# Kernel optimization log

Measured on AMD Instinct MI355X. Metric: run time of the kernel, lower is better.

## Reference

```python
import jax, jax.numpy as jnp
import numpy as np

CLF_LAMBDA = 1.0
SCENARIO_SCALES = (1.0, 1.2)


def setup_inputs() -> dict:
    key = jax.random.key(0)
    ks = jax.random.split(key, 20)
    B, N, H, NC = 65536, 16, 128, 2
    s_in = 1.0 / np.sqrt(N)
    s_h = 1.0 / np.sqrt(H)
    return {
        "x": jax.random.normal(ks[0], (B, N), jnp.float32),
        "V1_w": jax.random.normal(ks[1], (H, N), jnp.float32) * s_in,
        "V1_b": jax.random.normal(ks[2], (H,), jnp.float32) * 0.1,
        "V2_w": jax.random.normal(ks[3], (H, H), jnp.float32) * s_h,
        "V2_b": jax.random.normal(ks[4], (H,), jnp.float32) * 0.1,
        "K1a_w": jax.random.normal(ks[5], (H, N), jnp.float32) * s_in,
        "K1a_b": jax.random.normal(ks[6], (H,), jnp.float32) * 0.1,
        "K1b_w": jax.random.normal(ks[7], (N, H), jnp.float32) * s_h,
        "K1b_b": jax.random.normal(ks[8], (N,), jnp.float32) * 0.1,
        "K2a_w": jax.random.normal(ks[9], (H, N), jnp.float32) * s_in,
        "K2a_b": jax.random.normal(ks[10], (H,), jnp.float32) * 0.1,
        "K2b_w": jax.random.normal(ks[11], (N, H), jnp.float32) * s_h,
        "K2b_b": jax.random.normal(ks[12], (N,), jnp.float32) * 0.1,
        "A_dyn": jax.random.normal(ks[13], (N, N), jnp.float32) * s_in,
        "B_dyn": jax.random.normal(ks[14], (N, NC), jnp.float32) * s_in,
        "x_goal": jax.random.normal(ks[15], (N,), jnp.float32),
        "u_eq": jax.random.normal(ks[16], (NC, 1), jnp.float32),
    }


def _forward(x, V1_w, V1_b, V2_w, V2_b, K1a_w, K1a_b, K1b_w, K1b_b,
             K2a_w, K2a_b, K2b_w, K2b_b, A_dyn, B_dyn, x_goal, u_eq):
    # --- Lyapunov value + manual Jacobian (diag_embed(1-t^2)@W == row-scaling) ---
    t1 = jnp.tanh(x @ V1_w.T + V1_b)                       # [B,H]
    t2 = jnp.tanh(t1 @ V2_w.T + V2_b)                      # [B,H]
    V = 0.5 * jnp.sum(t2 * t2, axis=1)                     # [B]
    D1 = (1.0 - t1 * t1)[:, :, None] * V1_w                # [B,H,N]
    # (diag(1-t2^2) @ V2_w) @ D1, contracted without materializing [B,H,H]
    D2 = jnp.einsum('bh,hk,bkn->bhn', 1.0 - t2 * t2, V2_w, D1)  # [B,H,N]
    grad_V = jnp.einsum('bh,bhn->bn', t2, D2)[:, None, :]  # [B,1,N]

    # --- learned gains K = stack(K1,K2); u = -K (x - x_goal) + u_eq ---
    K1 = jnp.tanh(x @ K1a_w.T + K1a_b) @ K1b_w.T + K1b_b   # [B,N]
    K2 = jnp.tanh(x @ K2a_w.T + K2a_b) @ K2b_w.T + K2b_b   # [B,N]
    K = jnp.stack((K1, K2), axis=1)                        # [B,2,N]
    dx = x - x_goal                                        # [B,N]
    u = -jnp.einsum('bcn,bn->bc', K, dx)[:, :, None] + u_eq  # [B,2,1]

    # --- CLF decrease condition per scenario (linear control-affine dynamics) ---
    gV = grad_V[:, 0, :]                                   # [B,N]
    L_g_V = gV @ B_dyn                                     # [B,NC] (g is state-indep)
    Vdot = jnp.zeros((x.shape[0], 1, 1), x.dtype)
    for scale in SCENARIO_SCALES:
        f = scale * (x @ A_dyn.T)                          # [B,N]
        L_f_V = jnp.sum(gV * f, axis=1)[:, None, None]     # [B,1,1]
        LgVu = jnp.einsum('bc,bco->bo', L_g_V, u)[:, :, None]  # [B,1,1]
        Vdot = Vdot + jax.nn.relu(L_f_V + LgVu + CLF_LAMBDA * V[:, None, None])
    Vdot = Vdot / len(SCENARIO_SCALES)
    relaxation = jnp.zeros((1,), x.dtype)
    return u, relaxation, V, Vdot


def reference(x, V1_w, V1_b, V2_w, V2_b, K1a_w, K1a_b, K1b_w, K1b_b,
              K2a_w, K2a_b, K2b_w, K2b_b, A_dyn, B_dyn, x_goal, u_eq):
    return _forward(x, V1_w, V1_b, V2_w, V2_b, K1a_w, K1a_b, K1b_w, K1b_b,
                    K2a_w, K2a_b, K2b_w, K2b_b, A_dyn, B_dyn, x_goal, u_eq)
```

## Files before the change

### kernel.cpp

```cpp
#include <hip/hip_runtime.h>


typedef __attribute__((ext_vector_type(8))) short bf8_t;
typedef __attribute__((ext_vector_type(4))) float f4_t;
typedef __attribute__((ext_vector_type(4))) short s4_t;

#define MFMA16(a, b, c) __builtin_amdgcn_mfma_f32_16x16x32_bf16((a), (b), (c), 0, 0, 0)

__device__ __forceinline__ float fast_tanh(float v) {
    float e = __builtin_amdgcn_exp2f(v * 2.885390081777927f);
    return 1.0f - 2.0f * __builtin_amdgcn_rcpf(e + 1.0f);
}
__device__ __forceinline__ unsigned short bf16_of(float f) {
    union { float f; unsigned u; } v; v.f = f;
    return (unsigned short)((v.u + 0x8000u) >> 16);
}
__device__ __forceinline__ unsigned pk2(float a, float b) {
    union { float f; unsigned u; } va, vb; va.f = a; vb.f = b;
    return ((va.u + 0x8000u) >> 16) | ((vb.u + 0x8000u) & 0xFFFF0000u);
}
__device__ __forceinline__ float unbf(unsigned short s) {
    union { unsigned u; float f; } v; v.u = ((unsigned)s) << 16; return v.f;
}

__global__ void prep_weights(const float* __restrict__ V1_w,
                             const float* __restrict__ V2_w,
                             const float* __restrict__ K1a_w,
                             const float* __restrict__ K1b_w,
                             const float* __restrict__ K2a_w,
                             const float* __restrict__ K2b_w,
                             const float* __restrict__ A_dyn,
                             unsigned short* __restrict__ ws) {
    int i = blockIdx.x * 256 + threadIdx.x;
    if (i < 2048) {
        ws[i] = bf16_of(V1_w[i]);
        int k = i & 127;
        ws[2048 + i] = bf16_of(V1_w[k * 16 + (i >> 7)]);
        ws[36864 + i] = bf16_of(K1a_w[i]);
        ws[38912 + i] = bf16_of(K2a_w[i]);
        ws[40960 + i] = bf16_of(K1b_w[i]);
        ws[43008 + i] = bf16_of(K2b_w[i]);
    }
    if (i < 16384) {
        ws[4096 + i] = bf16_of(V2_w[i]);
        int k = i >> 7, h = i & 127;
        ws[20480 + i] = bf16_of(V2_w[h * 128 + k]);
    }
    if (i < 256) ws[45056 + i] = bf16_of(A_dyn[i]);
}

__device__ __forceinline__ bf8_t pack8(f4_t a, f4_t b) {
    union { bf8_t v; unsigned u[4]; } r;
    r.u[0] = pk2(a[0], a[1]); r.u[1] = pk2(a[2], a[3]);
    r.u[2] = pk2(b[0], b[1]); r.u[3] = pk2(b[2], b[3]);
    return r.v;
}

__global__ void __launch_bounds__(512) clf_mfma_kernel(
    const float* __restrict__ x,
    const float* __restrict__ V1_b, const float* __restrict__ V2_b,
    const float* __restrict__ K1a_b, const float* __restrict__ K1b_b,
    const float* __restrict__ K2a_b, const float* __restrict__ K2b_b,
    const float* __restrict__ B_dyn, const float* __restrict__ x_goal,
    const float* __restrict__ u_eq,
    const unsigned short* __restrict__ ws, float* __restrict__ out, int B) {
    extern __shared__ unsigned short sm[];
    unsigned short* V2s  = sm;
    unsigned short* V2Ts = sm + 16384;
    unsigned short* V1Ts = sm + 32768;
    unsigned short* K1bs = sm + 34816;
    unsigned short* K2bs = sm + 36864;
    const int lane = threadIdx.x & 63;
    const int wv = threadIdx.x >> 6;
    const int lr = lane & 15;
    const int g = lane >> 4;
    const int bb = (blockIdx.x * 8 + wv) * 16 + lr;
    unsigned short* bufA = sm + 38912 + wv * 4096;
    unsigned short* bufB = bufA + 2048;

    if (blockIdx.x == 0 && threadIdx.x == 0) out[2 * B] = 0.0f;

#pragma unroll
    for (int q = 0; q < 4; ++q) {
        int e = (q * 512 + threadIdx.x) * 8;
        int r = e >> 7;
        int d = e ^ ((r & 7) << 3);
        *reinterpret_cast<uint4*>(&V2s[d])  = *reinterpret_cast<const uint4*>(ws + 4096 + e);
        *reinterpret_cast<uint4*>(&V2Ts[d]) = *reinterpret_cast<const uint4*>(ws + 20480 + e);
    }
    {
        int t3 = threadIdx.x;
        if (t3 < 256) {
            int e = t3 * 8; int r = e >> 7; int d = e ^ ((r & 7) << 3);
            *reinterpret_cast<uint4*>(&V1Ts[d]) = *reinterpret_cast<const uint4*>(ws + 2048 + e);
            *reinterpret_cast<uint4*>(&K2bs[d]) = *reinterpret_cast<const uint4*>(ws + 43008 + e);
        } else {
            int e = (t3 - 256) * 8; int r = e >> 7; int d = e ^ ((r & 7) << 3);
            *reinterpret_cast<uint4*>(&K1bs[d]) = *reinterpret_cast<const uint4*>(ws + 40960 + e);
        }
    }
    __syncthreads();

    const unsigned short* wsV1 = ws;
    const unsigned short* wsK1a = ws + 36864;
    const unsigned short* wsK2a = ws + 38912;
    const unsigned short* wsA = ws + 45056;

    const int swz = (lr & 7) << 3;
    auto stA = [&](unsigned short* buf, int h0, unsigned lo, unsigned hi) {
        int idx = (lr * 128 + h0) ^ swz;
        uint2 v; v.x = lo; v.y = hi;
        *reinterpret_cast<uint2*>(buf + idx) = v;
    };
    auto ld8 = [&](const unsigned short* buf, int h0) -> bf8_t {
        int idx = (lr * 128 + h0) ^ swz;
        return *reinterpret_cast<const bf8_t*>(buf + idx);
    };
    auto ld4 = [&](const unsigned short* buf, int h0) -> s4_t {
        int idx = (lr * 128 + h0) ^ swz;
        return *reinterpret_cast<const s4_t*>(buf + idx);
    };
    auto ldW = [&](const unsigned short* Wt, int t, int c) -> bf8_t {
        int idx = ((t * 16 + lr) * 128 + c * 32 + g * 8) ^ swz;
        return *reinterpret_cast<const bf8_t*>(Wt + idx);
    };
    auto ldK = [&](const unsigned short* Wt, int c) -> bf8_t {
        int idx = (lr * 128 + c * 32 + g * 8) ^ swz;
        return *reinterpret_cast<const bf8_t*>(Wt + idx);
    };

    bf8_t xf = {0, 0, 0, 0, 0, 0, 0, 0};
    if (g < 2) {
        const float* xp = x + bb * 16 + g * 8;
        f4_t a = *reinterpret_cast<const f4_t*>(xp);
        f4_t b = *reinterpret_cast<const f4_t*>(xp + 4);
        xf = pack8(a, b);
    }

    auto actnet = [&](const unsigned short* wsW, const float* bias, unsigned short* dst) {
#pragma unroll
        for (int t = 0; t < 8; ++t) {
            bf8_t af = {0, 0, 0, 0, 0, 0, 0, 0};
            if (g < 2) af = *reinterpret_cast<const bf8_t*>(wsW + (t * 16 + lr) * 16 + g * 8);
            f4_t acc = {0.f, 0.f, 0.f, 0.f};
            acc = MFMA16(af, xf, acc);
            f4_t bs = *reinterpret_cast<const f4_t*>(bias + t * 16 + g * 4);
            float v0 = fast_tanh(acc[0] + bs[0]);
            float v1 = fast_tanh(acc[1] + bs[1]);
            float v2 = fast_tanh(acc[2] + bs[2]);
            float v3 = fast_tanh(acc[3] + bs[3]);
            stA(dst, t * 16 + g * 4, pk2(v0, v1), pk2(v2, v3));
        }
    };
    auto ldfrag = [&](const unsigned short* buf, bf8_t (&f)[4]) {
        f[0] = ld8(buf, 0 + g * 8); f[1] = ld8(buf, 32 + g * 8);
        f[2] = ld8(buf, 64 + g * 8); f[3] = ld8(buf, 96 + g * 8);
    };
    auto kmul = [&](const unsigned short* Wt, const bf8_t (&f)[4]) -> f4_t {
        f4_t za = {0.f, 0.f, 0.f, 0.f}, zb = {0.f, 0.f, 0.f, 0.f};
        za = MFMA16(ldK(Wt, 0), f[0], za);
        zb = MFMA16(ldK(Wt, 1), f[1], zb);
        za = MFMA16(ldK(Wt, 2), f[2], za);
        zb = MFMA16(ldK(Wt, 3), f[3], zb);
        f4_t k;
        k[0] = za[0] + zb[0]; k[1] = za[1] + zb[1];
        k[2] = za[2] + zb[2]; k[3] = za[3] + zb[3];
        return k;
    };

    actnet(wsK1a, K1a_b, bufA);
    actnet(wsK2a, K2a_b, bufB);
    bf8_t fragA[4], fragB[4];
    ldfrag(bufA, fragA);
    ldfrag(bufB, fragB);
    f4_t k1 = kmul(K1bs, fragA);
    f4_t k2 = kmul(K2bs, fragB);

    actnet(wsV1, V1_b, bufA);
    bf8_t t1f[4];
    ldfrag(bufA, t1f);

    float vsum = 0.f;
#pragma unroll
    for (int t = 0; t < 8; ++t) {
        f4_t za = {0.f, 0.f, 0.f, 0.f}, zb = {0.f, 0.f, 0.f, 0.f};
        za = MFMA16(ldW(V2s, t, 0), t1f[0], za);
        zb = MFMA16(ldW(V2s, t, 1), t1f[1], zb);
        za = MFMA16(ldW(V2s, t, 2), t1f[2], za);
        zb = MFMA16(ldW(V2s, t, 3), t1f[3], zb);
        f4_t bs = *reinterpret_cast<const f4_t*>(V2_b + t * 16 + g * 4);
        float s0, s1, s2v, s3;
        {
            float t2;
            t2 = fast_tanh(za[0] + zb[0] + bs[0]); vsum = fmaf(t2, t2, vsum); s0 = t2 * (1.f - t2 * t2);
            t2 = fast_tanh(za[1] + zb[1] + bs[1]); vsum = fmaf(t2, t2, vsum); s1 = t2 * (1.f - t2 * t2);
            t2 = fast_tanh(za[2] + zb[2] + bs[2]); vsum = fmaf(t2, t2, vsum); s2v = t2 * (1.f - t2 * t2);
            t2 = fast_tanh(za[3] + zb[3] + bs[3]); vsum = fmaf(t2, t2, vsum); s3 = t2 * (1.f - t2 * t2);
        }
        stA(bufB, t * 16 + g * 4, pk2(s0, s1), pk2(s2v, s3));
    }
    bf8_t s2f[4];
    ldfrag(bufB, s2f);

#pragma unroll
    for (int t = 0; t < 8; ++t) {
        f4_t za = {0.f, 0.f, 0.f, 0.f}, zb = {0.f, 0.f, 0.f, 0.f};
        za = MFMA16(ldW(V2Ts, t, 0), s2f[0], za);
        zb = MFMA16(ldW(V2Ts, t, 1), s2f[1], zb);
        za = MFMA16(ldW(V2Ts, t, 2), s2f[2], za);
        zb = MFMA16(ldW(V2Ts, t, 3), s2f[3], zb);
        s4_t tv = ld4(bufA, t * 16 + g * 4);
        float t0v = unbf((unsigned short)tv[0]);
        float t1v = unbf((unsigned short)tv[1]);
        float t2v = unbf((unsigned short)tv[2]);
        float t3v = unbf((unsigned short)tv[3]);
        float c0 = (za[0] + zb[0]) * (1.f - t0v * t0v);
        float c1 = (za[1] + zb[1]) * (1.f - t1v * t1v);
        float c2 = (za[2] + zb[2]) * (1.f - t2v * t2v);
        float c3 = (za[3] + zb[3]) * (1.f - t3v * t3v);
        stA(bufB, t * 16 + g * 4, pk2(c0, c1), pk2(c2, c3));
    }
    bf8_t cf[4];
    ldfrag(bufB, cf);

    f4_t gacc = kmul(V1Ts, cf);

    bf8_t afA = {0, 0, 0, 0, 0, 0, 0, 0};
    if (g < 2) afA = *reinterpret_cast<const bf8_t*>(wsA + lr * 16 + g * 8);
    f4_t fz = {0.f, 0.f, 0.f, 0.f};
    f4_t fac = MFMA16(afA, xf, fz);

    f4_t xv = *reinterpret_cast<const f4_t*>(x + bb * 16 + g * 4);
    f4_t xg = *reinterpret_cast<const f4_t*>(x_goal + g * 4);
    f4_t k1b = *reinterpret_cast<const f4_t*>(K1b_b + g * 4);
    f4_t k2b = *reinterpret_cast<const f4_t*>(K2b_b + g * 4);
    f4_t bd0 = *reinterpret_cast<const f4_t*>(B_dyn + g * 8);
    f4_t bd1 = *reinterpret_cast<const f4_t*>(B_dyn + g * 8 + 4);
    float up0 = 0.f, up1 = 0.f, Lf = 0.f;
#pragma unroll
    for (int r = 0; r < 4; ++r) {
        float dx = xv[r] - xg[r];
        up0 = fmaf(k1[r] + k1b[r], dx, up0);
        up1 = fmaf(k2[r] + k2b[r], dx, up1);
        Lf = fmaf(gacc[r], fac[r], Lf);
    }
    float Lg0 = gacc[0] * bd0[0] + gacc[1] * bd0[2] + gacc[2] * bd1[0] + gacc[3] * bd1[2];
    float Lg1 = gacc[0] * bd0[1] + gacc[1] * bd0[3] + gacc[2] * bd1[1] + gacc[3] * bd1[3];
    up0 += __shfl_xor(up0, 16); up0 += __shfl_xor(up0, 32);
    up1 += __shfl_xor(up1, 16); up1 += __shfl_xor(up1, 32);
    Lf += __shfl_xor(Lf, 16); Lf += __shfl_xor(Lf, 32);
    Lg0 += __shfl_xor(Lg0, 16); Lg0 += __shfl_xor(Lg0, 32);
    Lg1 += __shfl_xor(Lg1, 16); Lg1 += __shfl_xor(Lg1, 32);
    vsum += __shfl_xor(vsum, 16); vsum += __shfl_xor(vsum, 32);

    float u0 = u_eq[0] - up0;
    float u1 = u_eq[1] - up1;
    float V = 0.5f * vsum;
    float G = fmaf(Lg0, u0, fmaf(Lg1, u1, V));
    float Vd = 0.5f * (fmaxf(Lf + G, 0.f) + fmaxf(fmaf(1.2f, Lf, G), 0.f));

    if (g == 0) {
        float2 uo; uo.x = u0; uo.y = u1;
        *reinterpret_cast<float2*>(out + 2 * bb) = uo;
    } else if (g == 1) {
        out[2 * B + 1 + bb] = V;
    } else if (g == 2) {
        out[3 * B + 1 + bb] = Vd;
    }
}

extern "C" void kernel_launch(void* const* d_in, const int* in_sizes, int n_in,
                              void* d_out, int out_size, void* d_ws, size_t ws_size,
                              hipStream_t stream) {
    const float* x = (const float*)d_in[0];
    const float* V1_w = (const float*)d_in[1];
    const float* V1_b = (const float*)d_in[2];
    const float* V2_w = (const float*)d_in[3];
    const float* V2_b = (const float*)d_in[4];
    const float* K1a_w = (const float*)d_in[5];
    const float* K1a_b = (const float*)d_in[6];
    const float* K1b_w = (const float*)d_in[7];
    const float* K1b_b = (const float*)d_in[8];
    const float* K2a_w = (const float*)d_in[9];
    const float* K2a_b = (const float*)d_in[10];
    const float* K2b_w = (const float*)d_in[11];
    const float* K2b_b = (const float*)d_in[12];
    const float* A_dyn = (const float*)d_in[13];
    const float* B_dyn = (const float*)d_in[14];
    const float* x_goal = (const float*)d_in[15];
    const float* u_eq = (const float*)d_in[16];
    float* out = (float*)d_out;
    unsigned short* ws = (unsigned short*)d_ws;

    const int B = in_sizes[0] / 16;
    const size_t smem = 143360;
    (void)hipFuncSetAttribute(reinterpret_cast<const void*>(clf_mfma_kernel),
                              hipFuncAttributeMaxDynamicSharedMemorySize, (int)smem);
    prep_weights<<<64, 256, 0, stream>>>(V1_w, V2_w, K1a_w, K1b_w, K2a_w, K2b_w, A_dyn, ws);
    clf_mfma_kernel<<<512, 512, smem, stream>>>(
        x, V1_b, V2_b, K1a_b, K1b_b, K2a_b, K2b_b,
        B_dyn, x_goal, u_eq, ws, out, B);
}
```

Baseline: 38.32 us.

## Use 11 waves per block and read small K/V1T weights from global

```diff
diff --git a/kernel.cpp b/kernel.cpp
--- a/kernel.cpp
+++ b/kernel.cpp
@@ -56,7 +56,7 @@
     return r.v;
 }
 
-__global__ void __launch_bounds__(512) clf_mfma_kernel(
+__global__ void __launch_bounds__(704) clf_mfma_kernel(
     const float* __restrict__ x,
     const float* __restrict__ V1_b, const float* __restrict__ V2_b,
     const float* __restrict__ K1a_b, const float* __restrict__ K1b_b,
@@ -67,43 +67,37 @@
     extern __shared__ unsigned short sm[];
     unsigned short* V2s  = sm;
     unsigned short* V2Ts = sm + 16384;
-    unsigned short* V1Ts = sm + 32768;
-    unsigned short* K1bs = sm + 34816;
-    unsigned short* K2bs = sm + 36864;
     const int lane = threadIdx.x & 63;
     const int wv = threadIdx.x >> 6;
     const int lr = lane & 15;
     const int g = lane >> 4;
-    const int bb = (blockIdx.x * 8 + wv) * 16 + lr;
-    unsigned short* bufA = sm + 38912 + wv * 4096;
+    const int wgid = blockIdx.x * 11 + wv;
+    const int bb = wgid * 16 + lr;
+    unsigned short* bufA = sm + 32768 + wv * 4096;
     unsigned short* bufB = bufA + 2048;
 
     if (blockIdx.x == 0 && threadIdx.x == 0) out[2 * B] = 0.0f;
 
 #pragma unroll
-    for (int q = 0; q < 4; ++q) {
-        int e = (q * 512 + threadIdx.x) * 8;
-        int r = e >> 7;
-        int d = e ^ ((r & 7) << 3);
-        *reinterpret_cast<uint4*>(&V2s[d])  = *reinterpret_cast<const uint4*>(ws + 4096 + e);
-        *reinterpret_cast<uint4*>(&V2Ts[d]) = *reinterpret_cast<const uint4*>(ws + 20480 + e);
-    }
-    {
-        int t3 = threadIdx.x;
-        if (t3 < 256) {
-            int e = t3 * 8; int r = e >> 7; int d = e ^ ((r & 7) << 3);
-            *reinterpret_cast<uint4*>(&V1Ts[d]) = *reinterpret_cast<const uint4*>(ws + 2048 + e);
-            *reinterpret_cast<uint4*>(&K2bs[d]) = *reinterpret_cast<const uint4*>(ws + 43008 + e);
-        } else {
-            int e = (t3 - 256) * 8; int r = e >> 7; int d = e ^ ((r & 7) << 3);
-            *reinterpret_cast<uint4*>(&K1bs[d]) = *reinterpret_cast<const uint4*>(ws + 40960 + e);
+    for (int q = 0; q < 3; ++q) {
+        int idx = q * 704 + threadIdx.x;
+        if (idx < 2048) {
+            int e = idx * 8;
+            int r = e >> 7;
+            int d = e ^ ((r & 7) << 3);
+            *reinterpret_cast<uint4*>(&V2s[d])  = *reinterpret_cast<const uint4*>(ws + 4096 + e);
+            *reinterpret_cast<uint4*>(&V2Ts[d]) = *reinterpret_cast<const uint4*>(ws + 20480 + e);
         }
     }
     __syncthreads();
+    if (wgid * 16 >= B) return;
 
     const unsigned short* wsV1 = ws;
+    const unsigned short* wsV1T = ws + 2048;
     const unsigned short* wsK1a = ws + 36864;
     const unsigned short* wsK2a = ws + 38912;
+    const unsigned short* wsK1b = ws + 40960;
+    const unsigned short* wsK2b = ws + 43008;
     const unsigned short* wsA = ws + 45056;
 
     const int swz = (lr & 7) << 3;
@@ -122,10 +116,6 @@
     };
     auto ldW = [&](const unsigned short* Wt, int t, int c) -> bf8_t {
         int idx = ((t * 16 + lr) * 128 + c * 32 + g * 8) ^ swz;
-        return *reinterpret_cast<const bf8_t*>(Wt + idx);
-    };
-    auto ldK = [&](const unsigned short* Wt, int c) -> bf8_t {
-        int idx = (lr * 128 + c * 32 + g * 8) ^ swz;
         return *reinterpret_cast<const bf8_t*>(Wt + idx);
     };
 
@@ -156,12 +146,13 @@
         f[0] = ld8(buf, 0 + g * 8); f[1] = ld8(buf, 32 + g * 8);
         f[2] = ld8(buf, 64 + g * 8); f[3] = ld8(buf, 96 + g * 8);
     };
-    auto kmul = [&](const unsigned short* Wt, const bf8_t (&f)[4]) -> f4_t {
+    auto kmul = [&](const unsigned short* wsKb, const bf8_t (&f)[4]) -> f4_t {
+        const unsigned short* ar = wsKb + lr * 128 + g * 8;
         f4_t za = {0.f, 0.f, 0.f, 0.f}, zb = {0.f, 0.f, 0.f, 0.f};
-        za = MFMA16(ldK(Wt, 0), f[0], za);
-        zb = MFMA16(ldK(Wt, 1), f[1], zb);
-        za = MFMA16(ldK(Wt, 2), f[2], za);
-        zb = MFMA16(ldK(Wt, 3), f[3], zb);
+        za = MFMA16(*reinterpret_cast<const bf8_t*>(ar), f[0], za);
+        zb = MFMA16(*reinterpret_cast<const bf8_t*>(ar + 32), f[1], zb);
+        za = MFMA16(*reinterpret_cast<const bf8_t*>(ar + 64), f[2], za);
+        zb = MFMA16(*reinterpret_cast<const bf8_t*>(ar + 96), f[3], zb);
         f4_t k;
         k[0] = za[0] + zb[0]; k[1] = za[1] + zb[1];
         k[2] = za[2] + zb[2]; k[3] = za[3] + zb[3];
@@ -173,8 +164,8 @@
     bf8_t fragA[4], fragB[4];
     ldfrag(bufA, fragA);
     ldfrag(bufB, fragB);
-    f4_t k1 = kmul(K1bs, fragA);
-    f4_t k2 = kmul(K2bs, fragB);
+    f4_t k1 = kmul(wsK1b, fragA);
+    f4_t k2 = kmul(wsK2b, fragB);
 
     actnet(wsV1, V1_b, bufA);
     bf8_t t1f[4];
@@ -223,7 +214,7 @@
     bf8_t cf[4];
     ldfrag(bufB, cf);
 
-    f4_t gacc = kmul(V1Ts, cf);
+    f4_t gacc = kmul(wsV1T, cf);
 
     bf8_t afA = {0, 0, 0, 0, 0, 0, 0, 0};
     if (g < 2) afA = *reinterpret_cast<const bf8_t*>(wsA + lr * 16 + g * 8);
@@ -293,11 +284,13 @@
     unsigned short* ws = (unsigned short*)d_ws;
 
     const int B = in_sizes[0] / 16;
-    const size_t smem = 143360;
+    const size_t smem = 155648;
     (void)hipFuncSetAttribute(reinterpret_cast<const void*>(clf_mfma_kernel),
                               hipFuncAttributeMaxDynamicSharedMemorySize, (int)smem);
     prep_weights<<<64, 256, 0, stream>>>(V1_w, V2_w, K1a_w, K1b_w, K2a_w, K2b_w, A_dyn, ws);
-    clf_mfma_kernel<<<512, 512, smem, stream>>>(
+    const int waves = B / 16;
+    const int blocks = (waves + 10) / 11;
+    clf_mfma_kernel<<<blocks, 704, smem, stream>>>(
         x, V1_b, V2_b, K1a_b, K1b_b, K2a_b, K2b_b,
         B_dyn, x_goal, u_eq, ws, out, B);
 }
```

After: 45.17 us. +17.9%, slower.
